# Kernel optimization log

Hardware: AMD Instinct MI355X
Metric: run time of the kernel (lower is better)

Reference implementation:

```python
import math
import jax, jax.numpy as jnp
import numpy as np

B, L, DIM, H = 2, 2048, 1024, 16
D = DIM // H  # head_dim = 64
EPS = 1e-6


def setup_inputs() -> dict:
    key = jax.random.key(0)
    ks = jax.random.split(key, 5)
    s = 0.02
    return {
        "x": jax.random.normal(ks[0], (B, L, DIM), jnp.float32),
        "pe": jax.random.normal(ks[1], (B, 1, L, D // 2, 2, 2), jnp.float32),
        "w_qkv": jax.random.normal(ks[2], (DIM, 3 * DIM), jnp.float32) * s,
        "q_scale": jnp.ones((D,), jnp.float32),
        "k_scale": jnp.ones((D,), jnp.float32),
        "w_proj": jax.random.normal(ks[3], (DIM, DIM), jnp.float32) * s,
        "b_proj": jnp.zeros((DIM,), jnp.float32),
    }


def _rmsnorm(t, scale):
    # flax nnx.RMSNorm: x * rsqrt(mean(x^2) + eps) * scale, over last dim
    var = jnp.mean(jnp.square(t), axis=-1, keepdims=True)
    return t * jax.lax.rsqrt(var + EPS) * scale


def _apply_rope(t, pe):
    # t: [B,H,L,D]; pe: [B,1,L,D/2,2,2]
    t2 = t.reshape(*t.shape[:-1], D // 2, 1, 2)
    out = pe[..., 0] * t2[..., 0] + pe[..., 1] * t2[..., 1]  # [B,H,L,D/2,2]
    return out.reshape(t.shape)


def reference(x, pe, w_qkv, q_scale, k_scale, w_proj, b_proj):
    # fused QKV projection
    qkv = jnp.einsum('bld,de->ble', x, w_qkv)  # [B,L,3*DIM]
    qkv = qkv.reshape(B, L, 3, H, D).transpose(2, 0, 3, 1, 4)  # [3,B,H,L,D]
    q, k, v = qkv[0], qkv[1], qkv[2]
    # QK RMSNorm
    q = _rmsnorm(q, q_scale)
    k = _rmsnorm(k, k_scale)
    # RoPE via pe
    q = _apply_rope(q, pe)
    k = _apply_rope(k, pe)
    # scaled dot product attention
    scores = jnp.einsum('bhqd,bhkd->bhqk', q, k) / math.sqrt(D)
    attn = jax.nn.softmax(scores, axis=-1)
    o = jnp.einsum('bhqk,bhkd->bhqd', attn, v)  # [B,H,L,D]
    o = o.transpose(0, 2, 1, 3).reshape(B, L, DIM)  # B H L D -> B L (H D)
    # output projection
    return jnp.einsum('bld,de->ble', o, w_proj) + b_proj
```

## Files before the change

kernel.cpp:

```cpp
#include <hip/hip_runtime.h>
#include <math.h>

#define BB 2
#define LL 2048
#define DIMM 1024
#define HH 16
#define DD 64
#define QKV_N 3072

typedef unsigned short u16;
typedef unsigned int u32;
typedef __attribute__((ext_vector_type(8))) short short8;
typedef __attribute__((ext_vector_type(4))) float f32x4;

__device__ __forceinline__ float bf2f(u16 h) {
    unsigned u = ((unsigned)h) << 16;
    return __uint_as_float(u);
}
__device__ __forceinline__ u16 f2bf(float f) {
    unsigned u = __float_as_uint(f);
    u += 0x7fffu + ((u >> 16) & 1u);
    return (u16)(u >> 16);
}
__device__ __forceinline__ u32 pack_bf2(float lo, float hi) {
    u32 a = __float_as_uint(hi) + 0x8000u;
    u32 b = __float_as_uint(lo) + 0x8000u;
    return __builtin_amdgcn_perm(a, b, 0x07060302u);
}
__device__ __forceinline__ void gload16(const u16* g, u16* l) {
    __builtin_amdgcn_global_load_lds(
        (const __attribute__((address_space(1))) void*)g,
        (__attribute__((address_space(3))) void*)l, 16, 0, 0);
}

__global__ __launch_bounds__(256) void convx(
    const float* __restrict__ X, u16* __restrict__ Xb)
{
    int i = (blockIdx.x * 256 + threadIdx.x) * 8;
    float4 a = *(const float4*)&X[i];
    float4 b = *(const float4*)&X[i + 4];
    u16 t[8] = {f2bf(a.x), f2bf(a.y), f2bf(a.z), f2bf(a.w),
                f2bf(b.x), f2bf(b.y), f2bf(b.z), f2bf(b.w)};
    *(uint4*)&Xb[i] = *(uint4*)t;
}

__global__ __launch_bounds__(256) void convt(
    const float* __restrict__ W, u16* __restrict__ Wt, int K, int N)
{
    __shared__ u16 s[64][72];
    const int tid = threadIdx.x;
    const int k0 = blockIdx.x * 64, n0 = blockIdx.y * 64;
#pragma unroll
    for (int t = 0; t < 16; ++t) {
        int flat = t * 256 + tid;
        int kk = flat >> 6, nn = flat & 63;
        s[nn][kk] = f2bf(W[(size_t)(k0 + kk) * N + n0 + nn]);
    }
    __syncthreads();
#pragma unroll
    for (int t = 0; t < 2; ++t) {
        int chunk = t * 256 + tid;
        int nn = chunk >> 3, kc = chunk & 7;
        *(uint4*)&Wt[(size_t)(n0 + nn) * K + k0 + kc * 8] = *(uint4*)&s[nn][kc * 8];
    }
}

__global__ __launch_bounds__(256) void gemm_qkv(
    const u16* __restrict__ A, const u16* __restrict__ Bt,
    u16* __restrict__ C, u16* __restrict__ kp, u16* __restrict__ vp,
    const float* __restrict__ pe,
    const float* __restrict__ qs, const float* __restrict__ ks)
{
    __shared__ u16 smem[2 * 128 * 64];
    u16* sA = smem;
    u16* sB = smem + 128 * 64;

    const int tid = threadIdx.x;
    const int wave = tid >> 6, lane = tid & 63;
    const int mIdx = lane & 15, quad = lane >> 4;
    const int wr = wave >> 1, wc = wave & 1;
    const int m0 = blockIdx.y * 128, n0 = blockIdx.x * 128;
    const int N = QKV_N, K = DIMM;
    const int lr = lane >> 3, lc = lane & 7;

    f32x4 acc[4][4];
#pragma unroll
    for (int a = 0; a < 4; ++a)
#pragma unroll
        for (int b = 0; b < 4; ++b) acc[a][b] = (f32x4){0.f, 0.f, 0.f, 0.f};

    for (int k0 = 0; k0 < K; k0 += 64) {
#pragma unroll
        for (int j = 0; j < 4; ++j) {
            int r0 = 32 * wave + 8 * j + lr;
            int kc = 8 * (lc ^ (r0 & 7));
            gload16(&A[(size_t)(m0 + r0) * K + k0 + kc], &sA[(32 * wave + 8 * j) * 64]);
            gload16(&Bt[(size_t)(n0 + r0) * K + k0 + kc], &sB[(32 * wave + 8 * j) * 64]);
        }
        __syncthreads();
#pragma unroll
        for (int ks2 = 0; ks2 < 2; ++ks2) {
            short8 af[4], bfr[4];
#pragma unroll
            for (int mt = 0; mt < 4; ++mt) {
                int Ra = 64 * wr + 16 * mt + mIdx;
                af[mt] = *(const short8*)&sA[Ra * 64 + 8 * ((ks2 * 4 + quad) ^ (Ra & 7))];
            }
#pragma unroll
            for (int nt = 0; nt < 4; ++nt) {
                int Rb = 64 * wc + 16 * nt + mIdx;
                bfr[nt] = *(const short8*)&sB[Rb * 64 + 8 * ((ks2 * 4 + quad) ^ (Rb & 7))];
            }
#pragma unroll
            for (int mt = 0; mt < 4; ++mt)
#pragma unroll
                for (int nt = 0; nt < 4; ++nt)
                    acc[mt][nt] = __builtin_amdgcn_mfma_f32_16x16x32_bf16(
                        af[mt], bfr[nt], acc[mt][nt], 0, 0, 0);
        }
        __syncthreads();
    }

    if (n0 >= 2048) {
#pragma unroll
        for (int mt = 0; mt < 4; ++mt) {
            const int tl0 = 64 * wr + 16 * mt + 4 * quad;
#pragma unroll
            for (int nt = 0; nt < 4; ++nt) {
                const int d = 16 * nt + mIdx;
                const int lblk = ((wc * 2 + (tl0 >> 6)) * 4 + (d >> 4)) * 2
                                 + ((tl0 >> 5) & 1);
                const int ln = (d & 15) + 16 * ((tl0 >> 3) & 3);
                uint2 pr;
                pr.x = pack_bf2(acc[mt][nt][0], acc[mt][nt][1]);
                pr.y = pack_bf2(acc[mt][nt][2], acc[mt][nt][3]);
                *(uint2*)&smem[lblk * 512 + ln * 8 + (tl0 & 7)] = pr;
            }
        }
        __syncthreads();
        {
            const int b = m0 >> 11;
            const int h0 = (n0 - 2048) >> 6;
            const int ktb = (m0 & 2047) >> 6;
#pragma unroll
            for (int g2 = 0; g2 < 4; ++g2) {
                const int bh = b * 16 + h0 + (g2 >> 1);
                const int kt = ktb + (g2 & 1);
                u16* dst = vp + ((size_t)(bh * 32 + kt) * 8) * 512;
                const u16* src = &smem[g2 * 8 * 512];
#pragma unroll
                for (int ps = 0; ps < 2; ++ps) {
                    const int off = (ps * 256 + tid) * 8;
                    *(uint4*)&dst[off] = *(const uint4*)&src[off];
                }
            }
        }
    } else {
        const bool isq = (n0 < 1024);
        const float* scv = isq ? qs : ks;
        const float pre = isq ? 0.18033688011112042f : 1.0f;
        float scl[4];
#pragma unroll
        for (int nt = 0; nt < 4; ++nt) scl[nt] = scv[16 * nt + mIdx];

#pragma unroll
        for (int mt = 0; mt < 4; ++mt) {
#pragma unroll
            for (int r = 0; r < 4; ++r) {
                float s = 0.f;
#pragma unroll
                for (int nt = 0; nt < 4; ++nt) {
                    float a = acc[mt][nt][r];
                    s += a * a;
                }
                s += __shfl_xor(s, 1);
                s += __shfl_xor(s, 2);
                s += __shfl_xor(s, 4);
                s += __shfl_xor(s, 8);
                float rn = rsqrtf(s * (1.f / 64.f) + 1e-6f);
                const int tl = 64 * wr + 16 * mt + 4 * quad + r;
                const int R = m0 + tl;
                size_t peo = (size_t)R * 128;
#pragma unroll
                for (int nt = 0; nt < 4; ++nt) {
                    float v = acc[mt][nt][r] * rn * scl[nt];
                    float pp = __shfl_xor(v, 1);
                    float2 pw = *(const float2*)&pe[peo + 2 * (16 * nt + mIdx)];
                    float e  = (mIdx & 1) ? pp : v;
                    float od = (mIdx & 1) ? v : pp;
                    u16 val = f2bf((pw.x * e + pw.y * od) * pre);
                    if (isq) {
                        C[(size_t)R * N + n0 + 64 * wc + 16 * nt + mIdx] = val;
                    } else {
                        const int d = 16 * nt + mIdx;
                        const int lblk = ((wc * 2 + (tl >> 6)) * 4 + ((tl >> 4) & 3)) * 2
                                         + (d >> 5);
                        smem[lblk * 512 + ((tl & 15) + 16 * ((d >> 3) & 3)) * 8
                             + (d & 7)] = val;
                    }
                }
            }
        }
        if (!isq) {
            __syncthreads();
            const int b = m0 >> 11;
            const int h0 = (n0 - 1024) >> 6;
            const int ktb = (m0 & 2047) >> 6;
#pragma unroll
            for (int g2 = 0; g2 < 4; ++g2) {
                const int bh = b * 16 + h0 + (g2 >> 1);
                const int kt = ktb + (g2 & 1);
                u16* dst = kp + ((size_t)(bh * 32 + kt) * 8) * 512;
                const u16* src = &smem[g2 * 8 * 512];
#pragma unroll
                for (int ps = 0; ps < 2; ++ps) {
                    const int off = (ps * 256 + tid) * 8;
                    *(uint4*)&dst[off] = *(const uint4*)&src[off];
                }
            }
        }
    }
}

__global__ __launch_bounds__(256) void gemm_proj(
    const u16* __restrict__ A, const u16* __restrict__ Bt,
    const float* __restrict__ bias, float* __restrict__ C)
{
    __shared__ u16 sA[64 * 64];
    __shared__ u16 sB[128 * 64];

    const int tid = threadIdx.x;
    const int wave = tid >> 6, lane = tid & 63;
    const int mIdx = lane & 15, quad = lane >> 4;
    const int wr = wave >> 1, wc = wave & 1;
    const int m0 = blockIdx.y * 64, n0 = blockIdx.x * 128;
    const int N = DIMM, K = DIMM;
    const int lr = lane >> 3, lc = lane & 7;

    f32x4 acc[2][4];
#pragma unroll
    for (int a = 0; a < 2; ++a)
#pragma unroll
        for (int b = 0; b < 4; ++b) acc[a][b] = (f32x4){0.f, 0.f, 0.f, 0.f};

    for (int k0 = 0; k0 < K; k0 += 64) {
#pragma unroll
        for (int j = 0; j < 2; ++j) {
            int r0 = 16 * wave + 8 * j + lr;
            int kc = 8 * (lc ^ (r0 & 7));
            gload16(&A[(size_t)(m0 + r0) * K + k0 + kc], &sA[(16 * wave + 8 * j) * 64]);
        }
#pragma unroll
        for (int j = 0; j < 4; ++j) {
            int r0 = 32 * wave + 8 * j + lr;
            int kc = 8 * (lc ^ (r0 & 7));
            gload16(&Bt[(size_t)(n0 + r0) * K + k0 + kc], &sB[(32 * wave + 8 * j) * 64]);
        }
        __syncthreads();
#pragma unroll
        for (int ks2 = 0; ks2 < 2; ++ks2) {
            short8 af[2], bfr[4];
#pragma unroll
            for (int mt = 0; mt < 2; ++mt) {
                int Ra = 32 * wr + 16 * mt + mIdx;
                af[mt] = *(const short8*)&sA[Ra * 64 + 8 * ((ks2 * 4 + quad) ^ (Ra & 7))];
            }
#pragma unroll
            for (int nt = 0; nt < 4; ++nt) {
                int Rb = 64 * wc + 16 * nt + mIdx;
                bfr[nt] = *(const short8*)&sB[Rb * 64 + 8 * ((ks2 * 4 + quad) ^ (Rb & 7))];
            }
#pragma unroll
            for (int mt = 0; mt < 2; ++mt)
#pragma unroll
                for (int nt = 0; nt < 4; ++nt)
                    acc[mt][nt] = __builtin_amdgcn_mfma_f32_16x16x32_bf16(
                        af[mt], bfr[nt], acc[mt][nt], 0, 0, 0);
        }
        __syncthreads();
    }

#pragma unroll
    for (int mt = 0; mt < 2; ++mt)
#pragma unroll
        for (int r = 0; r < 4; ++r) {
            int row = m0 + 32 * wr + 16 * mt + quad * 4 + r;
#pragma unroll
            for (int nt = 0; nt < 4; ++nt) {
                int col = n0 + 64 * wc + 16 * nt + mIdx;
                C[(size_t)row * N + col] = acc[mt][nt][r] + bias[col];
            }
        }
}

__global__ __launch_bounds__(256, 2) void attn_mfma(
    const u16* __restrict__ qkv, const u16* __restrict__ kp,
    const u16* __restrict__ vp, u16* __restrict__ o)
{
    __shared__ u16 sP[128 * 64];

    const int tid = threadIdx.x;
    const int wave = tid >> 6;
    const int lane = tid & 63;
    const int mIdx = lane & 15;
    const int quad = lane >> 4;
    const int m7 = mIdx & 7;

    const int bid = ((blockIdx.x & 7) << 6) | (blockIdx.x >> 3);
    const int bh = bid >> 4;
    const int qt = bid & 15;
    const int b = bh >> 4, h = bh & 15;
    const int q0 = qt * 128;

    const u16* kbase = kp + (size_t)bh * 32 * 4096 + lane * 8;
    const u16* vbase = vp + (size_t)bh * 32 * 4096 + lane * 8;

    short8 aq[2][2];
#pragma unroll
    for (int g = 0; g < 2; ++g) {
        const u16* qrow = qkv + (size_t)b * LL * QKV_N + h * 64
                          + (size_t)(q0 + 32 * wave + 16 * g + mIdx) * QKV_N;
        aq[g][0] = *(const short8*)&qrow[quad * 8];
        aq[g][1] = *(const short8*)&qrow[32 + quad * 8];
    }

    const short8 bones = {(short)0x3F80, (short)0x3F80, (short)0x3F80, (short)0x3F80,
                          (short)0x3F80, (short)0x3F80, (short)0x3F80, (short)0x3F80};

    f32x4 Oacc[2][4];
    f32x4 lac[2];
#pragma unroll
    for (int g = 0; g < 2; ++g) {
        lac[g] = (f32x4){0.f, 0.f, 0.f, 0.f};
#pragma unroll
        for (int nb = 0; nb < 4; ++nb) Oacc[g][nb] = (f32x4){0.f, 0.f, 0.f, 0.f};
    }

    const int o0 = 8 * (quad ^ m7);
    const int o1 = 8 * ((quad + 4) ^ m7);
    u16* sPr0 = &sP[(32 * wave + mIdx) * 64];
    u16* sPr1 = &sP[(32 * wave + 16 + mIdx) * 64];

    short8 kfA[8], kfB[8], vf[8];

#pragma unroll
    for (int f = 0; f < 8; ++f) kfA[f] = *(const short8*)&kbase[f * 512];

    auto body = [&](short8* KC, short8* KN, int kt) {
        const size_t tb = (size_t)kt * 4096;
#pragma unroll
        for (int f = 0; f < 8; ++f) vf[f] = *(const short8*)&vbase[tb + f * 512];
        if (kt < 31) {
#pragma unroll
            for (int f = 0; f < 8; ++f) KN[f] = *(const short8*)&kbase[tb + 4096 + f * 512];
        }
        __builtin_amdgcn_sched_barrier(0);

#pragma unroll
        for (int nb = 0; nb < 4; ++nb) {
            const int pofs = (16 * nb + 4 * quad) ^ (8 * m7);
#pragma unroll
            for (int g = 0; g < 2; ++g) {
                f32x4 st = (f32x4){0.f, 0.f, 0.f, 0.f};
                st = __builtin_amdgcn_mfma_f32_16x16x32_bf16(KC[nb * 2 + 0], aq[g][0], st, 0, 0, 0);
                st = __builtin_amdgcn_mfma_f32_16x16x32_bf16(KC[nb * 2 + 1], aq[g][1], st, 0, 0, 0);
                float p0 = exp2f(st[0]), p1 = exp2f(st[1]);
                float p2 = exp2f(st[2]), p3 = exp2f(st[3]);
                uint2 wp;
                wp.x = pack_bf2(p0, p1);
                wp.y = pack_bf2(p2, p3);
                *(uint2*)&((g == 0 ? sPr0 : sPr1)[pofs]) = wp;
            }
        }
        short8 pa00 = *(const short8*)&sPr0[o0];
        short8 pa01 = *(const short8*)&sPr0[o1];
        short8 pa10 = *(const short8*)&sPr1[o0];
        short8 pa11 = *(const short8*)&sPr1[o1];

        lac[0] = __builtin_amdgcn_mfma_f32_16x16x32_bf16(pa00, bones, lac[0], 0, 0, 0);
        lac[0] = __builtin_amdgcn_mfma_f32_16x16x32_bf16(pa01, bones, lac[0], 0, 0, 0);
        lac[1] = __builtin_amdgcn_mfma_f32_16x16x32_bf16(pa10, bones, lac[1], 0, 0, 0);
        lac[1] = __builtin_amdgcn_mfma_f32_16x16x32_bf16(pa11, bones, lac[1], 0, 0, 0);

        __builtin_amdgcn_s_setprio(1);
#pragma unroll
        for (int nb = 0; nb < 4; ++nb) {
            Oacc[0][nb] = __builtin_amdgcn_mfma_f32_16x16x32_bf16(pa00, vf[nb * 2 + 0], Oacc[0][nb], 0, 0, 0);
            Oacc[0][nb] = __builtin_amdgcn_mfma_f32_16x16x32_bf16(pa01, vf[nb * 2 + 1], Oacc[0][nb], 0, 0, 0);
            Oacc[1][nb] = __builtin_amdgcn_mfma_f32_16x16x32_bf16(pa10, vf[nb * 2 + 0], Oacc[1][nb], 0, 0, 0);
            Oacc[1][nb] = __builtin_amdgcn_mfma_f32_16x16x32_bf16(pa11, vf[nb * 2 + 1], Oacc[1][nb], 0, 0, 0);
        }
        __builtin_amdgcn_s_setprio(0);
    };

    for (int kt2 = 0; kt2 < 16; ++kt2) {
        body(kfA, kfB, 2 * kt2);
        body(kfB, kfA, 2 * kt2 + 1);
    }

#pragma unroll
    for (int g = 0; g < 2; ++g)
#pragma unroll
        for (int r = 0; r < 4; ++r) {
            float linv = 1.f / lac[g][r];
            const int rowg = b * LL + q0 + 32 * wave + 16 * g + quad * 4 + r;
#pragma unroll
            for (int nb = 0; nb < 4; ++nb) {
                o[(size_t)rowg * DIMM + h * 64 + 16 * nb + mIdx] =
                    f2bf(Oacc[g][nb][r] * linv);
            }
        }
}

extern "C" void kernel_launch(void* const* d_in, const int* in_sizes, int n_in,
                              void* d_out, int out_size, void* d_ws, size_t ws_size,
                              hipStream_t stream) {
    const float* x       = (const float*)d_in[0];
    const float* pe      = (const float*)d_in[1];
    const float* w_qkv   = (const float*)d_in[2];
    const float* q_scale = (const float*)d_in[3];
    const float* k_scale = (const float*)d_in[4];
    const float* w_proj  = (const float*)d_in[5];
    const float* b_proj  = (const float*)d_in[6];
    float* out = (float*)d_out;

    char* ws = (char*)d_ws;
    u16* qkv    = (u16*)ws;  ws += (size_t)4096 * 3072 * 2;
    u16* o      = (u16*)ws;  ws += (size_t)4096 * 1024 * 2;
    u16* xb     = (u16*)ws;  ws += (size_t)4096 * 1024 * 2;
    u16* wqkvt  = (u16*)ws;  ws += (size_t)3072 * 1024 * 2;
    u16* wprojt = (u16*)ws;  ws += (size_t)1024 * 1024 * 2;
    u16* kpack  = (u16*)ws;  ws += (size_t)32 * 32 * 4096 * 2;
    u16* vpack  = (u16*)ws;  ws += (size_t)32 * 32 * 4096 * 2;

    convx<<<(4096 * 1024) / (256 * 8), 256, 0, stream>>>(x, xb);
    convt<<<dim3(1024 / 64, QKV_N / 64), 256, 0, stream>>>(w_qkv, wqkvt, DIMM, QKV_N);
    convt<<<dim3(1024 / 64, 1024 / 64), 256, 0, stream>>>(w_proj, wprojt, DIMM, DIMM);

    gemm_qkv<<<dim3(QKV_N / 128, (BB * LL) / 128), 256, 0, stream>>>(
        xb, wqkvt, qkv, kpack, vpack, pe, q_scale, k_scale);

    attn_mfma<<<BB * HH * (LL / 128), 256, 0, stream>>>(qkv, kpack, vpack, o);

    gemm_proj<<<dim3(DIMM / 128, (BB * LL) / 64), 256, 0, stream>>>(
        o, wprojt, b_proj, out);
}
```

Measured before the change: 236.7 us.

## Double-buffer LDS in QKV and projection GEMMs and remap blocks per XCD

```diff
diff --git a/kernel.cpp b/kernel.cpp
--- a/kernel.cpp
+++ b/kernel.cpp
@@ -71,15 +71,15 @@
     const float* __restrict__ pe,
     const float* __restrict__ qs, const float* __restrict__ ks)
 {
-    __shared__ u16 smem[2 * 128 * 64];
-    u16* sA = smem;
-    u16* sB = smem + 128 * 64;
+    __shared__ u16 smem[2 * 16384];
 
     const int tid = threadIdx.x;
     const int wave = tid >> 6, lane = tid & 63;
     const int mIdx = lane & 15, quad = lane >> 4;
     const int wr = wave >> 1, wc = wave & 1;
-    const int m0 = blockIdx.y * 128, n0 = blockIdx.x * 128;
+    const int xcd = blockIdx.x & 7, lid = blockIdx.x >> 3;
+    const int m0 = ((xcd & 3) * 8 + (lid & 7)) * 128;
+    const int n0 = ((xcd >> 2) * 12 + (lid >> 3)) * 128;
     const int N = QKV_N, K = DIMM;
     const int lr = lane >> 3, lc = lane & 7;
 
@@ -89,15 +89,25 @@
 #pragma unroll
         for (int b = 0; b < 4; ++b) acc[a][b] = (f32x4){0.f, 0.f, 0.f, 0.f};
 
-    for (int k0 = 0; k0 < K; k0 += 64) {
+    auto stage = [&](int buf, int k0) {
+        u16* sA = smem + buf * 16384;
+        u16* sB = sA + 8192;
 #pragma unroll
         for (int j = 0; j < 4; ++j) {
             int r0 = 32 * wave + 8 * j + lr;
-            int kc = 8 * (lc ^ (r0 & 7));
+            int kc = 8 * (lc ^ lr);
             gload16(&A[(size_t)(m0 + r0) * K + k0 + kc], &sA[(32 * wave + 8 * j) * 64]);
             gload16(&Bt[(size_t)(n0 + r0) * K + k0 + kc], &sB[(32 * wave + 8 * j) * 64]);
         }
-        __syncthreads();
+    };
+
+    stage(0, 0);
+    __syncthreads();
+    int cur = 0;
+    for (int t = 0; t < 16; ++t) {
+        if (t + 1 < 16) stage(cur ^ 1, (t + 1) * 64);
+        const u16* sA = smem + cur * 16384;
+        const u16* sB = sA + 8192;
 #pragma unroll
         for (int ks2 = 0; ks2 < 2; ++ks2) {
             short8 af[4], bfr[4];
@@ -119,6 +129,7 @@
                         af[mt], bfr[nt], acc[mt][nt], 0, 0, 0);
         }
         __syncthreads();
+        cur ^= 1;
     }
 
     if (n0 >= 2048) {
@@ -226,14 +237,15 @@
     const u16* __restrict__ A, const u16* __restrict__ Bt,
     const float* __restrict__ bias, float* __restrict__ C)
 {
-    __shared__ u16 sA[64 * 64];
-    __shared__ u16 sB[128 * 64];
+    __shared__ u16 smem[2 * 12288];
 
     const int tid = threadIdx.x;
     const int wave = tid >> 6, lane = tid & 63;
     const int mIdx = lane & 15, quad = lane >> 4;
     const int wr = wave >> 1, wc = wave & 1;
-    const int m0 = blockIdx.y * 64, n0 = blockIdx.x * 128;
+    const int xcd = blockIdx.x & 7, lid = blockIdx.x >> 3;
+    const int m0 = (xcd * 8 + (lid >> 3)) * 64;
+    const int n0 = (lid & 7) * 128;
     const int N = DIMM, K = DIMM;
     const int lr = lane >> 3, lc = lane & 7;
 
@@ -243,20 +255,30 @@
 #pragma unroll
         for (int b = 0; b < 4; ++b) acc[a][b] = (f32x4){0.f, 0.f, 0.f, 0.f};
 
-    for (int k0 = 0; k0 < K; k0 += 64) {
+    auto stage = [&](int buf, int k0) {
+        u16* sA = smem + buf * 12288;
+        u16* sB = sA + 4096;
 #pragma unroll
         for (int j = 0; j < 2; ++j) {
             int r0 = 16 * wave + 8 * j + lr;
-            int kc = 8 * (lc ^ (r0 & 7));
-            gload16(&A[(size_t)(m0 + r0) * K + k0 + kc], &sA[(16 * wave + 8 * j) * 64]);
+            gload16(&A[(size_t)(m0 + r0) * K + k0 + 8 * (lc ^ lr)],
+                    &sA[(16 * wave + 8 * j) * 64]);
         }
 #pragma unroll
         for (int j = 0; j < 4; ++j) {
             int r0 = 32 * wave + 8 * j + lr;
-            int kc = 8 * (lc ^ (r0 & 7));
-            gload16(&Bt[(size_t)(n0 + r0) * K + k0 + kc], &sB[(32 * wave + 8 * j) * 64]);
-        }
-        __syncthreads();
+            gload16(&Bt[(size_t)(n0 + r0) * K + k0 + 8 * (lc ^ lr)],
+                    &sB[(32 * wave + 8 * j) * 64]);
+        }
+    };
+
+    stage(0, 0);
+    __syncthreads();
+    int cur = 0;
+    for (int t = 0; t < 16; ++t) {
+        if (t + 1 < 16) stage(cur ^ 1, (t + 1) * 64);
+        const u16* sA = smem + cur * 12288;
+        const u16* sB = sA + 4096;
 #pragma unroll
         for (int ks2 = 0; ks2 < 2; ++ks2) {
             short8 af[2], bfr[4];
@@ -278,6 +300,7 @@
                         af[mt], bfr[nt], acc[mt][nt], 0, 0, 0);
         }
         __syncthreads();
+        cur ^= 1;
     }
 
 #pragma unroll
@@ -437,11 +460,10 @@
     convt<<<dim3(1024 / 64, QKV_N / 64), 256, 0, stream>>>(w_qkv, wqkvt, DIMM, QKV_N);
     convt<<<dim3(1024 / 64, 1024 / 64), 256, 0, stream>>>(w_proj, wprojt, DIMM, DIMM);
 
-    gemm_qkv<<<dim3(QKV_N / 128, (BB * LL) / 128), 256, 0, stream>>>(
+    gemm_qkv<<<768, 256, 0, stream>>>(
         xb, wqkvt, qkv, kpack, vpack, pe, q_scale, k_scale);
 
     attn_mfma<<<BB * HH * (LL / 128), 256, 0, stream>>>(qkv, kpack, vpack, o);
 
-    gemm_proj<<<dim3(DIMM / 128, (BB * LL) / 64), 256, 0, stream>>>(
-        o, wprojt, b_proj, out);
-}
+    gemm_proj<<<512, 256, 0, stream>>>(o, wprojt, b_proj, out);
+}
```

New measurement: 231.5 us. 1.02x faster.
